# Kernel tuning notes

Measured on AMD Instinct MI355X. Metric: run time of the kernel, lower is better.

The kernel has to match this reference:

```python
import jax, jax.numpy as jnp
import numpy as np

B = 65536   # batch
F = 256     # FeatureDim
E = 8       # experts_num
D = 64      # ExpertOutDim
EPS = 1e-5  # BatchNorm eps (eval mode: running stats)


def _bn(x, g, be, m, v):
    # BatchNorm1d in eval mode
    return (x - m) * jax.lax.rsqrt(v + EPS) * g + be


def setup_inputs() -> dict:
    key = jax.random.key(0)
    ks = jax.random.split(key, 40)
    r = lambda i, s: jax.random.normal(ks[i], s, dtype=jnp.float32) * 0.05
    u = lambda i, s: jax.random.uniform(ks[i], s, dtype=jnp.float32)
    return dict(
        signal_em=jax.random.normal(ks[0], (B, F), dtype=jnp.float32),
        muti_em=jax.random.normal(ks[1], (B, F), dtype=jnp.float32),
        similarity=jax.random.uniform(ks[2], (B,), dtype=jnp.float32),
        w=u(3, ()), b=u(4, ()),
        ps_W=r(5, (F, 256)), ps_b=r(6, (256,)), ps_g=u(7, (256,)), ps_be=r(8, (256,)), ps_m=r(9, (256,)), ps_v=u(10, (256,)) + 0.5,
        pm_W=r(11, (F, 256)), pm_b=r(12, (256,)), pm_g=u(13, (256,)), pm_be=r(14, (256,)), pm_m=r(15, (256,)), pm_v=u(16, (256,)) + 0.5,
        c1_W=r(17, (2 * F, 64)), c1_b=r(18, (64,)), c1_g=u(19, (64,)), c1_be=r(20, (64,)), c1_m=r(21, (64,)), c1_v=u(22, (64,)) + 0.5,
        c2_W=r(23, (64, 64)), c2_b=r(24, (64,)), c2_g=u(25, (64,)), c2_be=r(26, (64,)), c2_m=r(27, (64,)), c2_v=u(28, (64,)) + 0.5,
        c3_W=r(29, (64, 2)), c3_b=r(30, (2,)),
        e_W1=r(31, (E, 2 * F, 256)), e_b1=r(32, (E, 256)),
        e_W2=r(33, (E, 256, D)), e_b2=r(34, (E, D)),
        s_W1=r(35, (E, E)), s_b1=r(36, (E,)), s_W2=r(37, (E, E)), s_b2=r(38, (E,)),
    )


def reference(signal_em, muti_em, similarity, w, b,
              ps_W, ps_b, ps_g, ps_be, ps_m, ps_v,
              pm_W, pm_b, pm_g, pm_be, pm_m, pm_v,
              c1_W, c1_b, c1_g, c1_be, c1_m, c1_v,
              c2_W, c2_b, c2_g, c2_be, c2_m, c2_v,
              c3_W, c3_b,
              e_W1, e_b1, e_W2, e_b2,
              s_W1, s_b1, s_W2, s_b2):
    sim_weight = similarity[:, None] * w + b                        # [B,1]
    sig = jax.nn.relu(_bn(signal_em @ ps_W + ps_b, ps_g, ps_be, ps_m, ps_v))
    sig = sim_weight * sig
    mut = jax.nn.relu(_bn(muti_em @ pm_W + pm_b, pm_g, pm_be, pm_m, pm_v))
    temp = jnp.concatenate([sig, mut], axis=1)                      # [B, 512]

    # classifier head (dropout = identity in eval mode)
    h = jax.nn.relu(_bn(temp @ c1_W + c1_b, c1_g, c1_be, c1_m, c1_v))
    h = jax.nn.relu(_bn(h @ c2_W + c2_b, c2_g, c2_be, c2_m, c2_v))
    pre_score = h @ c3_W + c3_b                                     # [B,2]

    # all E experts as one batched GEMM (Expert_net has dropout p=0)
    eh = jax.nn.relu(jnp.einsum('bf,efh->beh', temp, e_W1) + e_b1)  # [B,E,256]
    eo = jax.nn.relu(jnp.einsum('beh,ehd->bed', eh, e_W2) + e_b2)   # [B,E,64]

    # SE-style gating: avg/max pool over expert-out dim (kernel==D -> scalar)
    att_ave = eo.mean(axis=-1)                                      # [B,E]
    att_max = eo.max(axis=-1)                                       # [B,E]
    senet = lambda x: jax.nn.gelu(x @ s_W1 + s_b1, approximate=False) @ s_W2 + s_b2
    wts = jax.nn.sigmoid(senet(att_ave) + senet(att_max))           # [B,E]

    gate_out = jnp.einsum('bed,be->bd', eo, wts)                    # [B,D]
    return (gate_out, pre_score)
```

## Files before the change

### kernel.cpp

```cpp
#include <hip/hip_runtime.h>
#include <math.h>

using u32 = unsigned int;
using u16 = unsigned short;
typedef __attribute__((ext_vector_type(4))) float f4;
typedef __attribute__((ext_vector_type(4))) u32 u4;
typedef __attribute__((ext_vector_type(2))) u32 u2;
typedef __attribute__((ext_vector_type(8))) __bf16 b8;

union U4B8 { u4 u; b8 b; };

__device__ __forceinline__ u16 f2b(float x) {
  u32 u = __float_as_uint(x);
  u32 r = (u + 0x7FFFu + ((u >> 16) & 1u)) >> 16;
  return (u16)r;
}
__device__ __forceinline__ u32 pack2(float a, float b) { return (u32)f2b(a) | ((u32)f2b(b) << 16); }
__device__ __forceinline__ f4 mfma16(b8 a, b8 b, f4 c) {
  return __builtin_amdgcn_mfma_f32_16x16x32_bf16(a, b, c, 0, 0, 0);
}

#define FENCE() asm volatile("" ::: "memory")
#define RAWBAR() do { FENCE(); __builtin_amdgcn_s_barrier(); FENCE(); __builtin_amdgcn_sched_barrier(0); } while (0)
#define VMW(nlit) do { asm volatile("s_waitcnt vmcnt(" nlit ")" ::: "memory"); __builtin_amdgcn_sched_barrier(0); } while (0)
#define LGKM0() do { asm volatile("s_waitcnt lgkmcnt(0)" ::: "memory"); __builtin_amdgcn_sched_barrier(0); } while (0)
#define LBAR() do { LGKM0(); __builtin_amdgcn_s_barrier(); FENCE(); __builtin_amdgcn_sched_barrier(0); } while (0)

template <int NB>
__device__ __forceinline__ void gstage(const u16* g, u16* l, int t) {
#pragma unroll
  for (int i = 0; i < NB; i += 8192) {
    __builtin_amdgcn_global_load_lds(
        (__attribute__((address_space(1))) u32*)(g + (i >> 1) + t * 8),
        (__attribute__((address_space(3))) u32*)(l + (i >> 1) + ((t >> 6) << 9)),
        16, 0, 0);
  }
}

__global__ void prep_kernel(
    const float* __restrict__ ps_W, const float* __restrict__ ps_b, const float* __restrict__ ps_g,
    const float* __restrict__ ps_be, const float* __restrict__ ps_m, const float* __restrict__ ps_v,
    const float* __restrict__ pm_W, const float* __restrict__ pm_b, const float* __restrict__ pm_g,
    const float* __restrict__ pm_be, const float* __restrict__ pm_m, const float* __restrict__ pm_v,
    const float* __restrict__ c1_W, const float* __restrict__ c1_b, const float* __restrict__ c1_g,
    const float* __restrict__ c1_be, const float* __restrict__ c1_m, const float* __restrict__ c1_v,
    const float* __restrict__ c2_W, const float* __restrict__ c2_b, const float* __restrict__ c2_g,
    const float* __restrict__ c2_be, const float* __restrict__ c2_m, const float* __restrict__ c2_v,
    u16* __restrict__ pst, u16* __restrict__ pmt,
    u16* __restrict__ c1t, u16* __restrict__ c2t, float* __restrict__ fold)
{
  int i0 = blockIdx.x * blockDim.x + threadIdx.x;
  int stride = gridDim.x * blockDim.x;
  for (int idx = i0; idx < 65536; idx += stride) {
    int s = idx >> 14; int rem = idx & 16383;
    int n = rem >> 6, q = rem & 63;
    int k = s * 64 + (q ^ ((n & 7) << 3));
    pst[idx] = f2b(ps_W[k * 256 + n]);
    pmt[idx] = f2b(pm_W[k * 256 + n]);
  }
  for (int idx = i0; idx < 64 * 512; idx += stride) {
    int n = idx >> 9, q = idx & 511;
    int k = q ^ ((n & 7) << 3);
    c1t[idx] = f2b(c1_W[k * 64 + n]);
  }
  for (int idx = i0; idx < 64 * 64; idx += stride) {
    int n = idx >> 6, k = idx & 63;
    c2t[idx] = f2b(c2_W[k * 64 + n]);
  }
  for (int idx = i0; idx < 256; idx += stride) {
    float a = ps_g[idx] * rsqrtf(ps_v[idx] + 1e-5f);
    fold[idx] = a; fold[256 + idx] = (ps_b[idx] - ps_m[idx]) * a + ps_be[idx];
    float a2 = pm_g[idx] * rsqrtf(pm_v[idx] + 1e-5f);
    fold[512 + idx] = a2; fold[768 + idx] = (pm_b[idx] - pm_m[idx]) * a2 + pm_be[idx];
  }
  for (int idx = i0; idx < 64; idx += stride) {
    float a = c1_g[idx] * rsqrtf(c1_v[idx] + 1e-5f);
    fold[1024 + idx] = a; fold[1088 + idx] = (c1_b[idx] - c1_m[idx]) * a + c1_be[idx];
    float a2 = c2_g[idx] * rsqrtf(c2_v[idx] + 1e-5f);
    fold[1152 + idx] = a2; fold[1216 + idx] = (c2_b[idx] - c2_m[idx]) * a2 + c2_be[idx];
  }
}

__global__ __launch_bounds__(512, 4) void k1_kernel(
    const float* __restrict__ sig, const float* __restrict__ mut,
    const float* __restrict__ simil, const float* __restrict__ wS, const float* __restrict__ bS,
    const u16* __restrict__ pst, const u16* __restrict__ pmt,
    const float* __restrict__ fold, u16* __restrict__ temp,
    const float* __restrict__ e_W1, const float* __restrict__ e_W2,
    u16* __restrict__ w1t, u16* __restrict__ w2t)
{
  extern __shared__ __align__(16) u16 smk[];
  const int t = threadIdx.x;
  if (blockIdx.y == 2) {
    int i0 = blockIdx.x * 512 + t;
    const int stride = 1024 * 512;
    for (int idx = i0; idx < 8 * 256 * 512; idx += stride) {
      int e = idx >> 17; int rem = idx & 131071;
      int s = rem >> 14; int rem2 = rem & 16383;
      int n = rem2 >> 6; int q = rem2 & 63;
      int k = s * 64 + (q ^ ((n & 7) << 3));
      w1t[idx] = f2b(e_W1[e * 131072 + k * 256 + n]);
    }
    for (int idx = i0; idx < 8 * 64 * 256; idx += stride) {
      int e = idx >> 14; int rem = idx & 16383;
      int d = rem >> 8; int q = rem & 255;
      int h = q ^ ((d & 7) << 3);
      w2t[idx] = f2b(e_W2[e * 16384 + h * 64 + d]);
    }
    return;
  }
  const int w = t >> 6, l = t & 63;
  const int lr = l & 15, lk = (l >> 4) * 8, lv = (l >> 4) * 4;
  const int xoru = (l & 7) << 3;
  const int rg = w >> 1, cg = w & 1;
  const int half = blockIdx.y;
  const float* X = half ? mut : sig;
  const u16* Wt = half ? pmt : pst;
  const int rb = blockIdx.x;
  const int rg0 = rb * 64;
  const f4 ZF = {0.f, 0.f, 0.f, 0.f};
  const int myrow = rg * 16 + lr;

  f4 xr[16];
  {
    const float* xp = X + (rg0 + myrow) * 256 + lk;
#pragma unroll
    for (int c = 0; c < 8; ++c) {
      xr[2 * c]     = *(const f4*)(xp + c * 32);
      xr[2 * c + 1] = *(const f4*)(xp + c * 32 + 4);
    }
  }
  float swv = 1.f;
  if (half == 0) swv = simil[rg0 + myrow] * wS[0] + bS[0];
  gstage<32768>(Wt, smk, t);
  b8 af[8];
#pragma unroll
  for (int c = 0; c < 8; ++c) {
    U4B8 tmp;
    tmp.u[0] = pack2(xr[2 * c][0], xr[2 * c][1]);
    tmp.u[1] = pack2(xr[2 * c][2], xr[2 * c][3]);
    tmp.u[2] = pack2(xr[2 * c + 1][0], xr[2 * c + 1][1]);
    tmp.u[3] = pack2(xr[2 * c + 1][2], xr[2 * c + 1][3]);
    af[c] = tmp.b;
  }

  f4 acc[8];
#pragma unroll
  for (int i = 0; i < 8; ++i) acc[i] = ZF;

#define K1P(P, STG) do { \
    VMW("0"); RAWBAR(); \
    STG; \
    __builtin_amdgcn_s_setprio(1); \
    _Pragma("unroll") for (int kk = 0; kk < 2; ++kk) { \
      b8 bf[8]; \
      _Pragma("unroll") for (int nf = 0; nf < 8; ++nf) \
        bf[nf] = *(const b8*)(smk + ((P) & 1) * 16384 + (cg * 128 + nf * 16 + lr) * 64 + ((kk * 32 + lk) ^ xoru)); \
      _Pragma("unroll") for (int nf = 0; nf < 8; ++nf) \
        acc[nf] = mfma16(bf[nf], af[(P) * 2 + kk], acc[nf]); \
    } \
    __builtin_amdgcn_s_setprio(0); \
  } while (0)

  K1P(0, gstage<32768>(Wt + 16384, smk + 16384, t));
  K1P(1, gstage<32768>(Wt + 32768, smk, t));
  K1P(2, gstage<32768>(Wt + 49152, smk + 16384, t));
  K1P(3, (void)0);
#undef K1P

#pragma unroll
  for (int nf = 0; nf < 8; ++nf) {
    int col = cg * 128 + nf * 16 + lv;
    const f4 al = *(const f4*)(fold + half * 512 + col);
    const f4 be = *(const f4*)(fold + half * 512 + 256 + col);
    float v0 = fmaxf(acc[nf][0] * al[0] + be[0], 0.f) * swv;
    float v1 = fmaxf(acc[nf][1] * al[1] + be[1], 0.f) * swv;
    float v2 = fmaxf(acc[nf][2] * al[2] + be[2], 0.f) * swv;
    float v3 = fmaxf(acc[nf][3] * al[3] + be[3], 0.f) * swv;
    u2 pv; pv[0] = pack2(v0, v1); pv[1] = pack2(v2, v3);
    int st = col >> 6;
    int kin = col & 63;
    int q = kin ^ ((myrow & 7) << 3);
    *(u2*)(smk + st * 4096 + myrow * 64 + q) = pv;
  }
  LBAR();
  {
    u16* dst = temp + (rb >> 1) * 65536 + half * 32768 + (rb & 1) * 4096;
#pragma unroll
    for (int st = 0; st < 4; ++st) {
      u4 v = *(const u4*)(smk + st * 4096 + t * 8);
      *(u4*)(dst + st * 8192 + t * 8) = v;
    }
  }
}

__global__ __launch_bounds__(512, 2) void k2_kernel(
    u16* __restrict__ temp, const u16* __restrict__ w1t, const u16* __restrict__ w2t,
    const u16* __restrict__ c1t, const u16* __restrict__ c2t,
    const float* __restrict__ fold,
    const float* __restrict__ c3W, const float* __restrict__ c3B,
    const float* __restrict__ eb1, const float* __restrict__ eb2,
    const float* __restrict__ sW1, const float* __restrict__ sB1,
    const float* __restrict__ sW2, const float* __restrict__ sB2,
    float* __restrict__ outp)
{
  extern __shared__ __align__(16) u16 sm[];
  u16* smW  = sm;
  u16* smE  = sm + 32768;
  u16* smR2 = sm + 49152;
  float* attA  = (float*)(sm + 65536);
  float* attM  = attA + 1024;
  float* wtsb  = attM + 1024;
  float* c3sm  = wtsb + 1024;
  float* eb1sm = c3sm + 136;
  float* eb2sm = eb1sm + 2048;

  const int t = threadIdx.x, w = t >> 6, l = t & 63;
  const int lr = l & 15, lk = (l >> 4) * 8, lv = (l >> 4) * 4;
  const int xoru = (l & 7) << 3;
  const int rg = w >> 1, cg = w & 1;
  const int rg0 = blockIdx.x * 128;
  const f4 ZF = {0.f, 0.f, 0.f, 0.f};
  u16* tempE = temp + blockIdx.x * 65536;

  b8 af[16][2];

#define AFLOAD(R) { \
    _Pragma("unroll") for (int c8 = 0; c8 < 8; ++c8) { \
      _Pragma("unroll") for (int mi = 0; mi < 2; ++mi) \
        af[(R) * 8 + c8][mi] = *(const b8*)(smE + (c8 >> 1) * 8192 + (rg * 32 + mi * 16 + lr) * 64 + ((((c8 & 1) * 32) + lk) ^ xoru)); \
    } }

  {
    for (int z = t; z < 2048; z += 512) attA[z] = 0.f;
    f4 rEb1 = *(const f4*)(eb1 + t * 4);
    f4 rEb2 = ZF; if (t < 128) rEb2 = *(const f4*)(eb2 + t * 4);
    float rC3 = 0.f; if (t < 128) rC3 = c3W[t]; else if (t < 130) rC3 = c3B[t - 128];
    u4 rC2 = *(const u4*)(c2t + (t >> 3) * 64 + (t & 7) * 8);

    gstage<65536>(tempE, smE, t);
    gstage<65536>(c1t, smW, t);
    *(f4*)(eb1sm + t * 4) = rEb1;
    if (t < 128) *(f4*)(eb2sm + t * 4) = rEb2;
    if (t < 130) c3sm[t] = rC3;
    VMW("8"); RAWBAR();
    AFLOAD(0);
    asm volatile("s_waitcnt lgkmcnt(0)" ::: "memory");
    RAWBAR();
    gstage<65536>(tempE + 32768, smE, t);
    VMW("8"); RAWBAR();
    f4 ah[2][2] = {{ZF, ZF}, {ZF, ZF}};
#define HPART(R) { \
    __builtin_amdgcn_s_setprio(1); \
    _Pragma("unroll") for (int c8 = 0; c8 < 8; ++c8) { \
      _Pragma("unroll") for (int nf = 0; nf < 2; ++nf) { \
        b8 ch = *(const b8*)(smW + (cg * 32 + nf * 16 + lr) * 512 + ((((R) * 8 + c8) * 32 + lk) ^ xoru)); \
        _Pragma("unroll") for (int mi = 0; mi < 2; ++mi) \
          ah[nf][mi] = mfma16(ch, af[(R) * 8 + c8][mi], ah[nf][mi]); \
      } } \
    __builtin_amdgcn_s_setprio(0); }
    HPART(0)
    VMW("0"); RAWBAR();
    AFLOAD(1);
    HPART(1)
#undef HPART
    asm volatile("s_waitcnt lgkmcnt(0)" ::: "memory");
    RAWBAR();
    u16* h1b = smE;
    u16* c2sm = smR2;
    u16* h2b = smR2 + 4608;
#pragma unroll
    for (int nf = 0; nf < 2; ++nf) {
      int col = cg * 32 + nf * 16 + lv;
      const f4 av1 = *(const f4*)(fold + 1024 + col);
      const f4 bv1 = *(const f4*)(fold + 1088 + col);
#pragma unroll
      for (int mi = 0; mi < 2; ++mi) {
        int row = rg * 32 + mi * 16 + lr;
        u2 pv;
        pv[0] = pack2(fmaxf(ah[nf][mi][0] * av1[0] + bv1[0], 0.f), fmaxf(ah[nf][mi][1] * av1[1] + bv1[1], 0.f));
        pv[1] = pack2(fmaxf(ah[nf][mi][2] * av1[2] + bv1[2], 0.f), fmaxf(ah[nf][mi][3] * av1[3] + bv1[3], 0.f));
        *(u2*)(h1b + row * 72 + col) = pv;
      }
    }
    *(u4*)(c2sm + (t >> 3) * 72 + (t & 7) * 8) = rC2;
    LBAR();
    f4 a2[2][2] = {{ZF, ZF}, {ZF, ZF}};
#pragma unroll
    for (int kk = 0; kk < 2; ++kk) {
      b8 hf[2], cf[2];
#pragma unroll
      for (int mi = 0; mi < 2; ++mi)
        hf[mi] = *(const b8*)(h1b + (rg * 32 + mi * 16 + lr) * 72 + kk * 32 + lk);
#pragma unroll
      for (int nf = 0; nf < 2; ++nf)
        cf[nf] = *(const b8*)(c2sm + (cg * 32 + nf * 16 + lr) * 72 + kk * 32 + lk);
#pragma unroll
      for (int mi = 0; mi < 2; ++mi)
#pragma unroll
        for (int nf = 0; nf < 2; ++nf)
          a2[mi][nf] = mfma16(cf[nf], hf[mi], a2[mi][nf]);
    }
#pragma unroll
    for (int nf = 0; nf < 2; ++nf) {
      int col = cg * 32 + nf * 16 + lv;
      const f4 av2 = *(const f4*)(fold + 1152 + col);
      const f4 bv2 = *(const f4*)(fold + 1216 + col);
#pragma unroll
      for (int mi = 0; mi < 2; ++mi) {
        int row = rg * 32 + mi * 16 + lr;
        u2 pv;
        pv[0] = pack2(fmaxf(a2[mi][nf][0] * av2[0] + bv2[0], 0.f), fmaxf(a2[mi][nf][1] * av2[1] + bv2[1], 0.f));
        pv[1] = pack2(fmaxf(a2[mi][nf][2] * av2[2] + bv2[2], 0.f), fmaxf(a2[mi][nf][3] * av2[3] + bv2[3], 0.f));
        *(u2*)(h2b + row * 72 + col) = pv;
      }
    }
    LBAR();
    if (t < 256) {
      int row = t >> 1, c = t & 1;
      float s_ = c3sm[128 + c];
#pragma unroll
      for (int j = 0; j < 8; ++j) {
        u4 hv = *(const u4*)(h2b + row * 72 + j * 8);
#pragma unroll
        for (int q = 0; q < 4; ++q) {
          float lo = __uint_as_float(hv[q] << 16);
          float hi = __uint_as_float(hv[q] & 0xffff0000u);
          s_ += lo * c3sm[(j * 8 + q * 2) * 2 + c];
          s_ += hi * c3sm[(j * 8 + q * 2 + 1) * 2 + c];
        }
      }
      outp[4194304 + (rg0 + row) * 2 + c] = s_;
    }
    RAWBAR();
    gstage<32768>(w1t, smW, t);
  }

#define MPH(P, NW, ...) do { \
    VMW(NW); RAWBAR(); \
    __VA_ARGS__; \
    __builtin_amdgcn_s_setprio(1); \
    _Pragma("unroll") for (int kk = 0; kk < 2; ++kk) { \
      b8 bfA[4], bfB[4]; \
      _Pragma("unroll") for (int nf = 0; nf < 4; ++nf) \
        bfA[nf] = *(const b8*)(smW + ((P) & 1) * 16384 + (cg * 64 + nf * 16 + lr) * 64 + ((kk * 32 + lk) ^ xoru)); \
      _Pragma("unroll") for (int nf = 0; nf < 4; ++nf) \
        bfB[nf] = *(const b8*)(smW + ((P) & 1) * 16384 + 8192 + (cg * 64 + nf * 16 + lr) * 64 + ((kk * 32 + lk) ^ xoru)); \
      _Pragma("unroll") for (int nf = 0; nf < 4; ++nf) \
        _Pragma("unroll") for (int mi = 0; mi < 2; ++mi) \
          acc[nf][mi] = mfma16(bfA[nf], af[(P) * 2 + kk][mi], acc[nf][mi]); \
      _Pragma("unroll") for (int nf = 0; nf < 4; ++nf) \
        _Pragma("unroll") for (int mi = 0; mi < 2; ++mi) \
          acc[4 + nf][mi] = mfma16(bfB[nf], af[(P) * 2 + kk][mi], acc[4 + nf][mi]); \
    } \
    __builtin_amdgcn_s_setprio(0); \
  } while (0)

#define EHEPI(E, H, DST) { \
    _Pragma("unroll") for (int nf = 0; nf < 4; ++nf) { \
      int colL = cg * 64 + nf * 16 + lv; \
      const f4 bv = *(const f4*)(eb1sm + (E) * 256 + (H) * 128 + colL); \
      _Pragma("unroll") for (int mi = 0; mi < 2; ++mi) { \
        int row = rg * 32 + mi * 16 + lr; \
        f4 a_ = acc[(H) * 4 + nf][mi]; \
        u2 pv; \
        pv[0] = pack2(fmaxf(a_[0] + bv[0], 0.f), fmaxf(a_[1] + bv[1], 0.f)); \
        pv[1] = pack2(fmaxf(a_[2] + bv[2], 0.f), fmaxf(a_[3] + bv[3], 0.f)); \
        *(u2*)((DST) + row * 128 + (colL ^ xoru)) = pv; \
      } } }

#define G2ALL() do { \
    __builtin_amdgcn_s_setprio(1); \
    _Pragma("unroll") for (int kq = 0; kq < 8; ++kq) { \
      const u16* ebase = (kq < 4) ? smE : (smW + 16384); \
      b8 wf[2], ef[2]; \
      _Pragma("unroll") for (int nf = 0; nf < 2; ++nf) \
        wf[nf] = *(const b8*)(smR2 + (cg * 32 + nf * 16 + lr) * 256 + ((kq * 32 + lk) ^ xoru)); \
      _Pragma("unroll") for (int mi = 0; mi < 2; ++mi) \
        ef[mi] = *(const b8*)(ebase + (rg * 32 + mi * 16 + lr) * 128 + ((((kq & 3) * 32) + lk) ^ xoru)); \
      _Pragma("unroll") for (int mi = 0; mi < 2; ++mi) \
        _Pragma("unroll") for (int nf = 0; nf < 2; ++nf) \
          e2[mi][nf] = mfma16(wf[nf], ef[mi], e2[mi][nf]); \
    } \
    __builtin_amdgcn_s_setprio(0); \
  } while (0)

#define EXPERT(E, NWP0, NWG2) { \
    const u16* w1E = w1t + (E) * 131072; \
    f4 acc[8][2]; \
    _Pragma("unroll") for (int nf = 0; nf < 8; ++nf) \
      _Pragma("unroll") for (int mi = 0; mi < 2; ++mi) acc[nf][mi] = ZF; \
    MPH(0, NWP0, gstage<32768>(w1E + 1 * 16384, smW + 16384, t)); \
    MPH(1, "0",  gstage<32768>(w1E + 2 * 16384, smW, t)); \
    MPH(2, "0",  gstage<32768>(w1E + 3 * 16384, smW + 16384, t)); \
    MPH(3, "0",  gstage<32768>(w1E + 4 * 16384, smW, t)); \
    MPH(4, "0",  gstage<32768>(w1E + 5 * 16384, smW + 16384, t)); \
    MPH(5, "0",  gstage<32768>(w1E + 6 * 16384, smW, t)); \
    MPH(6, "0",  { gstage<32768>(w1E + 7 * 16384, smW + 16384, t); \
                   gstage<32768>(w2t + (E) * 16384, smR2, t); }); \
    MPH(7, "4",  { if ((E) < 7) gstage<32768>(w1t + ((E) + 1) * 131072, smW, t); }); \
    EHEPI(E, 0, smE) \
    RAWBAR();  \
    EHEPI(E, 1, smW + 16384) \
    VMW(NWG2); LBAR();  \
    f4 e2[2][2]; \
    e2[0][0] = ZF; e2[0][1] = ZF; e2[1][0] = ZF; e2[1][1] = ZF; \
    G2ALL(); \
     \
    _Pragma("unroll") for (int mi = 0; mi < 2; ++mi) { \
      int row = rg * 32 + mi * 16 + lr; \
      float s_ = 0.f, mx = 0.f; \
      _Pragma("unroll") for (int nf = 0; nf < 2; ++nf) { \
        int d0 = cg * 32 + nf * 16 + lv; \
        const f4 bv2 = *(const f4*)(eb2sm + (E) * 64 + d0); \
        float v0 = fmaxf(e2[mi][nf][0] + bv2[0], 0.f); \
        float v1 = fmaxf(e2[mi][nf][1] + bv2[1], 0.f); \
        float v2 = fmaxf(e2[mi][nf][2] + bv2[2], 0.f); \
        float v3 = fmaxf(e2[mi][nf][3] + bv2[3], 0.f); \
        s_ += v0 + v1 + v2 + v3; \
        mx = fmaxf(mx, fmaxf(fmaxf(v0, v1), fmaxf(v2, v3))); \
        u2 pv; pv[0] = pack2(v0, v1); pv[1] = pack2(v2, v3); \
        *(u2*)(tempE + (E) * 8192 + row * 64 + d0) = pv; \
      } \
      s_ += __shfl_xor(s_, 16); s_ += __shfl_xor(s_, 32); \
      mx = fmaxf(mx, __shfl_xor(mx, 16)); mx = fmaxf(mx, __shfl_xor(mx, 32)); \
      if (l < 16) { \
        atomicAdd(attA + row * 8 + (E), s_); \
        atomicMax((unsigned int*)(attM + row * 8 + (E)), __float_as_uint(mx)); \
      } \
    } \
  }

  EXPERT(0, "0", "4")
  EXPERT(1, "4", "4")
  EXPERT(2, "4", "4")
  EXPERT(3, "4", "4")
  EXPERT(4, "4", "4")
  EXPERT(5, "4", "4")
  EXPERT(6, "4", "4")
  EXPERT(7, "4", "0")
#undef EXPERT
#undef MPH
#undef EHEPI
#undef G2ALL

  VMW("0");
  LBAR();
  if (t < 128) {
    float xa[8], xm[8], ga[8], gm[8];
#pragma unroll
    for (int j = 0; j < 8; ++j) {
      xa[j] = attA[t * 8 + j] * 0.015625f;
      xm[j] = attM[t * 8 + j];
    }
#pragma unroll
    for (int j = 0; j < 8; ++j) {
      float a1 = sB1[j], a2 = sB1[j];
#pragma unroll
      for (int i = 0; i < 8; ++i) { float wv = sW1[i * 8 + j]; a1 += xa[i] * wv; a2 += xm[i] * wv; }
      ga[j] = 0.5f * a1 * (1.f + erff(a1 * 0.70710678118654752f));
      gm[j] = 0.5f * a2 * (1.f + erff(a2 * 0.70710678118654752f));
    }
#pragma unroll
    for (int j = 0; j < 8; ++j) {
      float o1 = sB2[j], o2 = sB2[j];
#pragma unroll
      for (int i = 0; i < 8; ++i) { float wv = sW2[i * 8 + j]; o1 += ga[i] * wv; o2 += gm[i] * wv; }
      float z = o1 + o2;
      wtsb[t * 8 + j] = 1.f / (1.f + expf(-z));
    }
  }
  LBAR();
  {
    int grow = t >> 2, gd0 = (t & 3) * 16;
    float wv[8];
#pragma unroll
    for (int e2_ = 0; e2_ < 8; ++e2_) wv[e2_] = wtsb[grow * 8 + e2_];
    float g[16];
#pragma unroll
    for (int j = 0; j < 16; ++j) g[j] = 0.f;
#pragma unroll
    for (int e2_ = 0; e2_ < 8; ++e2_) {
      const u16* wsE = tempE + e2_ * 8192 + grow * 64 + gd0;
      u4 qa = *(const u4*)(wsE); u4 qb = *(const u4*)(wsE + 8);
#pragma unroll
      for (int q = 0; q < 4; ++q) {
        g[2 * q + 0] += wv[e2_] * __uint_as_float(qa[q] << 16);
        g[2 * q + 1] += wv[e2_] * __uint_as_float(qa[q] & 0xffff0000u);
        g[8 + 2 * q + 0] += wv[e2_] * __uint_as_float(qb[q] << 16);
        g[8 + 2 * q + 1] += wv[e2_] * __uint_as_float(qb[q] & 0xffff0000u);
      }
    }
    float* op = outp + (rg0 + grow) * 64 + gd0;
    f4 o0 = {g[0], g[1], g[2], g[3]}, o1 = {g[4], g[5], g[6], g[7]};
    f4 o2 = {g[8], g[9], g[10], g[11]}, o3 = {g[12], g[13], g[14], g[15]};
    *(f4*)op = o0; *(f4*)(op + 4) = o1; *(f4*)(op + 8) = o2; *(f4*)(op + 12) = o3;
  }
}

extern "C" void kernel_launch(void* const* d_in, const int* in_sizes, int n_in,
                              void* d_out, int out_size, void* d_ws, size_t ws_size,
                              hipStream_t stream) {
  const float* signal = (const float*)d_in[0];
  const float* muti   = (const float*)d_in[1];
  const float* simil  = (const float*)d_in[2];
  const float* wS     = (const float*)d_in[3];
  const float* bS     = (const float*)d_in[4];
  const float* ps_W = (const float*)d_in[5];  const float* ps_b = (const float*)d_in[6];
  const float* ps_g = (const float*)d_in[7];  const float* ps_be = (const float*)d_in[8];
  const float* ps_m = (const float*)d_in[9];  const float* ps_v = (const float*)d_in[10];
  const float* pm_W = (const float*)d_in[11]; const float* pm_b = (const float*)d_in[12];
  const float* pm_g = (const float*)d_in[13]; const float* pm_be = (const float*)d_in[14];
  const float* pm_m = (const float*)d_in[15]; const float* pm_v = (const float*)d_in[16];
  const float* c1_W = (const float*)d_in[17]; const float* c1_b = (const float*)d_in[18];
  const float* c1_g = (const float*)d_in[19]; const float* c1_be = (const float*)d_in[20];
  const float* c1_m = (const float*)d_in[21]; const float* c1_v = (const float*)d_in[22];
  const float* c2_W = (const float*)d_in[23]; const float* c2_b = (const float*)d_in[24];
  const float* c2_g = (const float*)d_in[25]; const float* c2_be = (const float*)d_in[26];
  const float* c2_m = (const float*)d_in[27]; const float* c2_v = (const float*)d_in[28];
  const float* c3_W = (const float*)d_in[29]; const float* c3_b = (const float*)d_in[30];
  const float* e_W1 = (const float*)d_in[31]; const float* e_b1 = (const float*)d_in[32];
  const float* e_W2 = (const float*)d_in[33]; const float* e_b2 = (const float*)d_in[34];
  const float* s_W1 = (const float*)d_in[35]; const float* s_b1 = (const float*)d_in[36];
  const float* s_W2 = (const float*)d_in[37]; const float* s_b2 = (const float*)d_in[38];

  char* ws = (char*)d_ws;
  u16* temp = (u16*)ws;
  u16* w1t  = (u16*)(ws + 67108864);
  u16* w2t  = (u16*)(ws + 69206016);
  u16* pst  = (u16*)(ws + 69468160);
  u16* pmt  = (u16*)(ws + 69599232);
  u16* c1t  = (u16*)(ws + 69730304);
  u16* c2t  = (u16*)(ws + 69795840);
  float* fold = (float*)(ws + 69804032);
  float* outp = (float*)d_out;

  prep_kernel<<<dim3(256), dim3(256), 0, stream>>>(
      ps_W, ps_b, ps_g, ps_be, ps_m, ps_v, pm_W, pm_b, pm_g, pm_be, pm_m, pm_v,
      c1_W, c1_b, c1_g, c1_be, c1_m, c1_v, c2_W, c2_b, c2_g, c2_be, c2_m, c2_v,
      pst, pmt, c1t, c2t, fold);
  k1_kernel<<<dim3(1024, 3), dim3(512), 65536, stream>>>(
      signal, muti, simil, wS, bS, pst, pmt, fold, temp, e_W1, e_W2, w1t, w2t);
  k2_kernel<<<dim3(512), dim3(512), 154144, stream>>>(
      temp, w1t, w2t, c1t, c2t, fold, c3_W, c3_b, e_b1, e_b2, s_W1, s_b1, s_W2, s_b2, outp);
}
```

Measured before the change: 261.7 us.

## Shrink k2 to 64-row 256-thread blocks with smaller LDS footprint

Restructures the main expert kernel from 128-row, 512-thread blocks using about 154KB of LDS to 64-row, 256-thread blocks using about 72KB, doubling the grid to 1024 blocks. The temp layout, the w1t swizzle layout and the staging step sizes change to match. All phases now share a single LDS region, and expert biases are read from global memory instead of LDS. The aim is more resident blocks per CU and better latency hiding. In exchange, the cross-expert prefetch overlap and the multi-stage vmcnt pipelining are dropped (every phase waits for vmcnt 0), and each block re-reads the expert weights for only half as many rows.

```diff
diff --git a/kernel.cpp b/kernel.cpp
--- a/kernel.cpp
+++ b/kernel.cpp
@@ -26,10 +26,10 @@
 #define LGKM0() do { asm volatile("s_waitcnt lgkmcnt(0)" ::: "memory"); __builtin_amdgcn_sched_barrier(0); } while (0)
 #define LBAR() do { LGKM0(); __builtin_amdgcn_s_barrier(); FENCE(); __builtin_amdgcn_sched_barrier(0); } while (0)
 
-template <int NB>
+template <int NB, int STEP>
 __device__ __forceinline__ void gstage(const u16* g, u16* l, int t) {
 #pragma unroll
-  for (int i = 0; i < NB; i += 8192) {
+  for (int i = 0; i < NB; i += STEP) {
     __builtin_amdgcn_global_load_lds(
         (__attribute__((address_space(1))) u32*)(g + (i >> 1) + t * 8),
         (__attribute__((address_space(3))) u32*)(l + (i >> 1) + ((t >> 6) << 9)),
@@ -96,9 +96,10 @@
     const int stride = 1024 * 512;
     for (int idx = i0; idx < 8 * 256 * 512; idx += stride) {
       int e = idx >> 17; int rem = idx & 131071;
-      int s = rem >> 14; int rem2 = rem & 16383;
-      int n = rem2 >> 6; int q = rem2 & 63;
-      int k = s * 64 + (q ^ ((n & 7) << 3));
+      int S = rem >> 13; int rem2 = rem & 8191;
+      int nl = rem2 >> 6; int q = rem2 & 63;
+      int n = (S & 1) * 128 + nl;
+      int k = (S >> 1) * 64 + (q ^ ((nl & 7) << 3));
       w1t[idx] = f2b(e_W1[e * 131072 + k * 256 + n]);
     }
     for (int idx = i0; idx < 8 * 64 * 256; idx += stride) {
@@ -132,7 +133,7 @@
   }
   float swv = 1.f;
   if (half == 0) swv = simil[rg0 + myrow] * wS[0] + bS[0];
-  gstage<32768>(Wt, smk, t);
+  gstage<32768, 8192>(Wt, smk, t);
   b8 af[8];
 #pragma unroll
   for (int c = 0; c < 8; ++c) {
@@ -148,9 +149,9 @@
 #pragma unroll
   for (int i = 0; i < 8; ++i) acc[i] = ZF;
 
-#define K1P(P, STG) do { \
+#define K1P(P, ...) do { \
     VMW("0"); RAWBAR(); \
-    STG; \
+    __VA_ARGS__; \
     __builtin_amdgcn_s_setprio(1); \
     _Pragma("unroll") for (int kk = 0; kk < 2; ++kk) { \
       b8 bf[8]; \
@@ -162,9 +163,9 @@
     __builtin_amdgcn_s_setprio(0); \
   } while (0)
 
-  K1P(0, gstage<32768>(Wt + 16384, smk + 16384, t));
-  K1P(1, gstage<32768>(Wt + 32768, smk, t));
-  K1P(2, gstage<32768>(Wt + 49152, smk + 16384, t));
+  K1P(0, (gstage<32768, 8192>(Wt + 16384, smk + 16384, t)));
+  K1P(1, (gstage<32768, 8192>(Wt + 32768, smk, t)));
+  K1P(2, (gstage<32768, 8192>(Wt + 49152, smk + 16384, t)));
   K1P(3, (void)0);
 #undef K1P
 
@@ -185,16 +186,16 @@
   }
   LBAR();
   {
-    u16* dst = temp + (rb >> 1) * 65536 + half * 32768 + (rb & 1) * 4096;
+    u16* dst = temp + rb * 32768 + half * 16384;
 #pragma unroll
     for (int st = 0; st < 4; ++st) {
       u4 v = *(const u4*)(smk + st * 4096 + t * 8);
-      *(u4*)(dst + st * 8192 + t * 8) = v;
-    }
-  }
-}
-
-__global__ __launch_bounds__(512, 2) void k2_kernel(
+      *(u4*)(dst + st * 4096 + t * 8) = v;
+    }
+  }
+}
+
+__global__ __launch_bounds__(256, 2) void k2_kernel(
     u16* __restrict__ temp, const u16* __restrict__ w1t, const u16* __restrict__ w2t,
     const u16* __restrict__ c1t, const u16* __restrict__ c2t,
     const float* __restrict__ fold,
@@ -206,69 +207,61 @@
 {
   extern __shared__ __align__(16) u16 sm[];
   u16* smW  = sm;
-  u16* smE  = sm + 32768;
-  u16* smR2 = sm + 49152;
-  float* attA  = (float*)(sm + 65536);
-  float* attM  = attA + 1024;
-  float* wtsb  = attM + 1024;
-  float* c3sm  = wtsb + 1024;
-  float* eb1sm = c3sm + 136;
-  float* eb2sm = eb1sm + 2048;
+  float* attA = (float*)(sm + 32768);
+  float* attM = attA + 512;
+  float* wtsb = attM + 512;
+  float* c3sm = wtsb + 512;
 
   const int t = threadIdx.x, w = t >> 6, l = t & 63;
   const int lr = l & 15, lk = (l >> 4) * 8, lv = (l >> 4) * 4;
   const int xoru = (l & 7) << 3;
   const int rg = w >> 1, cg = w & 1;
-  const int rg0 = blockIdx.x * 128;
+  const int rg0 = blockIdx.x * 64;
   const f4 ZF = {0.f, 0.f, 0.f, 0.f};
-  u16* tempE = temp + blockIdx.x * 65536;
+  u16* tempE = temp + blockIdx.x * 32768;
 
   b8 af[16][2];
 
 #define AFLOAD(R) { \
     _Pragma("unroll") for (int c8 = 0; c8 < 8; ++c8) { \
       _Pragma("unroll") for (int mi = 0; mi < 2; ++mi) \
-        af[(R) * 8 + c8][mi] = *(const b8*)(smE + (c8 >> 1) * 8192 + (rg * 32 + mi * 16 + lr) * 64 + ((((c8 & 1) * 32) + lk) ^ xoru)); \
+        af[(R) * 8 + c8][mi] = *(const b8*)(smW + (R) * 16384 + (c8 >> 1) * 4096 + (rg * 32 + mi * 16 + lr) * 64 + ((((c8 & 1) * 32) + lk) ^ xoru)); \
     } }
 
   {
-    for (int z = t; z < 2048; z += 512) attA[z] = 0.f;
-    f4 rEb1 = *(const f4*)(eb1 + t * 4);
-    f4 rEb2 = ZF; if (t < 128) rEb2 = *(const f4*)(eb2 + t * 4);
+    for (int z = t; z < 1024; z += 256) attA[z] = 0.f;
     float rC3 = 0.f; if (t < 128) rC3 = c3W[t]; else if (t < 130) rC3 = c3B[t - 128];
-    u4 rC2 = *(const u4*)(c2t + (t >> 3) * 64 + (t & 7) * 8);
-
-    gstage<65536>(tempE, smE, t);
-    gstage<65536>(c1t, smW, t);
-    *(f4*)(eb1sm + t * 4) = rEb1;
-    if (t < 128) *(f4*)(eb2sm + t * 4) = rEb2;
+    u4 rC2a = *(const u4*)(c2t + (t >> 3) * 64 + (t & 7) * 8);
+    u4 rC2b = *(const u4*)(c2t + ((t + 256) >> 3) * 64 + ((t + 256) & 7) * 8);
+
+    gstage<32768, 4096>(tempE, smW, t);
+    gstage<32768, 4096>(tempE + 16384, smW + 16384, t);
     if (t < 130) c3sm[t] = rC3;
     VMW("8"); RAWBAR();
     AFLOAD(0);
-    asm volatile("s_waitcnt lgkmcnt(0)" ::: "memory");
-    RAWBAR();
-    gstage<65536>(tempE + 32768, smE, t);
-    VMW("8"); RAWBAR();
+    VMW("0");
+    LGKM0(); RAWBAR();
+    AFLOAD(1);
+    LGKM0(); RAWBAR();
+    gstage<65536, 4096>(c1t, smW, t);
+    VMW("0"); RAWBAR();
     f4 ah[2][2] = {{ZF, ZF}, {ZF, ZF}};
-#define HPART(R) { \
-    __builtin_amdgcn_s_setprio(1); \
-    _Pragma("unroll") for (int c8 = 0; c8 < 8; ++c8) { \
-      _Pragma("unroll") for (int nf = 0; nf < 2; ++nf) { \
-        b8 ch = *(const b8*)(smW + (cg * 32 + nf * 16 + lr) * 512 + ((((R) * 8 + c8) * 32 + lk) ^ xoru)); \
-        _Pragma("unroll") for (int mi = 0; mi < 2; ++mi) \
-          ah[nf][mi] = mfma16(ch, af[(R) * 8 + c8][mi], ah[nf][mi]); \
-      } } \
-    __builtin_amdgcn_s_setprio(0); }
-    HPART(0)
-    VMW("0"); RAWBAR();
-    AFLOAD(1);
-    HPART(1)
-#undef HPART
-    asm volatile("s_waitcnt lgkmcnt(0)" ::: "memory");
-    RAWBAR();
-    u16* h1b = smE;
-    u16* c2sm = smR2;
-    u16* h2b = smR2 + 4608;
+    __builtin_amdgcn_s_setprio(1);
+#pragma unroll
+    for (int c8 = 0; c8 < 16; ++c8) {
+#pragma unroll
+      for (int nf = 0; nf < 2; ++nf) {
+        b8 ch = *(const b8*)(smW + (cg * 32 + nf * 16 + lr) * 512 + ((c8 * 32 + lk) ^ xoru));
+#pragma unroll
+        for (int mi = 0; mi < 2; ++mi)
+          ah[nf][mi] = mfma16(ch, af[c8][mi], ah[nf][mi]);
+      }
+    }
+    __builtin_amdgcn_s_setprio(0);
+    LGKM0(); RAWBAR();
+    u16* h1b  = smW;
+    u16* c2sm = smW + 4608;
+    u16* h2b  = smW + 9216;
 #pragma unroll
     for (int nf = 0; nf < 2; ++nf) {
       int col = cg * 32 + nf * 16 + lv;
@@ -283,7 +276,8 @@
         *(u2*)(h1b + row * 72 + col) = pv;
       }
     }
-    *(u4*)(c2sm + (t >> 3) * 72 + (t & 7) * 8) = rC2;
+    *(u4*)(c2sm + (t >> 3) * 72 + (t & 7) * 8) = rC2a;
+    *(u4*)(c2sm + ((t + 256) >> 3) * 72 + ((t + 256) & 7) * 8) = rC2b;
     LBAR();
     f4 a2[2][2] = {{ZF, ZF}, {ZF, ZF}};
 #pragma unroll
@@ -316,7 +310,7 @@
       }
     }
     LBAR();
-    if (t < 256) {
+    if (t < 128) {
       int row = t >> 1, c = t & 1;
       float s_ = c3sm[128 + c];
 #pragma unroll
@@ -333,86 +327,106 @@
       outp[4194304 + (rg0 + row) * 2 + c] = s_;
     }
     RAWBAR();
-    gstage<32768>(w1t, smW, t);
-  }
-
-#define MPH(P, NW, ...) do { \
-    VMW(NW); RAWBAR(); \
+    gstage<32768, 4096>(w1t, smW, t);
+  }
+
+#define MPH(P, ...) do { \
+    VMW("0"); RAWBAR(); \
     __VA_ARGS__; \
     __builtin_amdgcn_s_setprio(1); \
     _Pragma("unroll") for (int kk = 0; kk < 2; ++kk) { \
-      b8 bfA[4], bfB[4]; \
-      _Pragma("unroll") for (int nf = 0; nf < 4; ++nf) \
-        bfA[nf] = *(const b8*)(smW + ((P) & 1) * 16384 + (cg * 64 + nf * 16 + lr) * 64 + ((kk * 32 + lk) ^ xoru)); \
-      _Pragma("unroll") for (int nf = 0; nf < 4; ++nf) \
-        bfB[nf] = *(const b8*)(smW + ((P) & 1) * 16384 + 8192 + (cg * 64 + nf * 16 + lr) * 64 + ((kk * 32 + lk) ^ xoru)); \
-      _Pragma("unroll") for (int nf = 0; nf < 4; ++nf) \
-        _Pragma("unroll") for (int mi = 0; mi < 2; ++mi) \
-          acc[nf][mi] = mfma16(bfA[nf], af[(P) * 2 + kk][mi], acc[nf][mi]); \
-      _Pragma("unroll") for (int nf = 0; nf < 4; ++nf) \
-        _Pragma("unroll") for (int mi = 0; mi < 2; ++mi) \
-          acc[4 + nf][mi] = mfma16(bfB[nf], af[(P) * 2 + kk][mi], acc[4 + nf][mi]); \
+      b8 bf[8]; \
+      _Pragma("unroll") for (int nf = 0; nf < 8; ++nf) \
+        bf[nf] = *(const b8*)(smW + ((P) & 1) * 16384 + cg * 8192 + (nf * 16 + lr) * 64 + ((kk * 32 + lk) ^ xoru)); \
+      _Pragma("unroll") for (int nf = 0; nf < 8; ++nf) \
+        acc[nf] = mfma16(bf[nf], af[(P) * 2 + kk], acc[nf]); \
     } \
     __builtin_amdgcn_s_setprio(0); \
   } while (0)
 
-#define EHEPI(E, H, DST) { \
-    _Pragma("unroll") for (int nf = 0; nf < 4; ++nf) { \
-      int colL = cg * 64 + nf * 16 + lv; \
-      const f4 bv = *(const f4*)(eb1sm + (E) * 256 + (H) * 128 + colL); \
-      _Pragma("unroll") for (int mi = 0; mi < 2; ++mi) { \
-        int row = rg * 32 + mi * 16 + lr; \
-        f4 a_ = acc[(H) * 4 + nf][mi]; \
+#define G32(SRC, DST) gstage<32768, 4096>((SRC), (DST), t)
+
+#define EXPERT(E) { \
+    const u16* w1E = w1t + (E) * 131072; \
+    f4 acc[8]; \
+    _Pragma("unroll") for (int nf = 0; nf < 8; ++nf) acc[nf] = ZF; \
+    MPH(0, G32(w1E + 1 * 16384, smW + 16384)); \
+    MPH(1, G32(w1E + 2 * 16384, smW)); \
+    MPH(2, G32(w1E + 3 * 16384, smW + 16384)); \
+    MPH(3, G32(w1E + 4 * 16384, smW)); \
+    MPH(4, G32(w1E + 5 * 16384, smW + 16384)); \
+    MPH(5, G32(w1E + 6 * 16384, smW)); \
+    MPH(6, G32(w1E + 7 * 16384, smW + 16384)); \
+    MPH(7, G32(w2t + (E) * 16384, smW)); \
+    VMW("0"); RAWBAR();  \
+     \
+    _Pragma("unroll") for (int nf = 0; nf < 8; ++nf) { \
+      int col = cg * 128 + nf * 16 + lv; \
+      const f4 bv = *(const f4*)(eb1 + (E) * 256 + col); \
+      int row = rg * 32 + lr;   \
+      (void)row; \
+      _Pragma("unroll") for (int mi = 0; mi < 1; ++mi) { } \
+      { \
+        int r0 = rg * 32 + lr; \
+        f4 a_ = acc[nf]; \
         u2 pv; \
         pv[0] = pack2(fmaxf(a_[0] + bv[0], 0.f), fmaxf(a_[1] + bv[1], 0.f)); \
         pv[1] = pack2(fmaxf(a_[2] + bv[2], 0.f), fmaxf(a_[3] + bv[3], 0.f)); \
-        *(u2*)((DST) + row * 128 + (colL ^ xoru)) = pv; \
-      } } }
-
-#define G2ALL() do { \
+        *(u2*)(smW + 16384 + r0 * 256 + (col ^ xoru)) = pv; \
+      } \
+    } \
+    LBAR(); \
+  }
+
+#undef EXPERT
+#define EXPERT(E) { \
+    const u16* w1E = w1t + (E) * 131072; \
+    f4 acc[8][2]; \
+    _Pragma("unroll") for (int nf = 0; nf < 8; ++nf) \
+      _Pragma("unroll") for (int mi = 0; mi < 2; ++mi) acc[nf][mi] = ZF; \
+    MPH2(0, G32(w1E + 1 * 16384, smW + 16384)); \
+    MPH2(1, G32(w1E + 2 * 16384, smW)); \
+    MPH2(2, G32(w1E + 3 * 16384, smW + 16384)); \
+    MPH2(3, G32(w1E + 4 * 16384, smW)); \
+    MPH2(4, G32(w1E + 5 * 16384, smW + 16384)); \
+    MPH2(5, G32(w1E + 6 * 16384, smW)); \
+    MPH2(6, G32(w1E + 7 * 16384, smW + 16384)); \
+    MPH2(7, G32(w2t + (E) * 16384, smW)); \
+    VMW("0"); RAWBAR();  \
+     \
+    _Pragma("unroll") for (int nf = 0; nf < 8; ++nf) { \
+      int col = cg * 128 + nf * 16 + lv; \
+      const f4 bv = *(const f4*)(eb1 + (E) * 256 + col); \
+      _Pragma("unroll") for (int mi = 0; mi < 2; ++mi) { \
+        int row = rg * 32 + mi * 16 + lr; \
+        f4 a_ = acc[nf][mi]; \
+        u2 pv; \
+        pv[0] = pack2(fmaxf(a_[0] + bv[0], 0.f), fmaxf(a_[1] + bv[1], 0.f)); \
+        pv[1] = pack2(fmaxf(a_[2] + bv[2], 0.f), fmaxf(a_[3] + bv[3], 0.f)); \
+        *(u2*)(smW + 16384 + row * 256 + (col ^ xoru)) = pv; \
+      } } \
+    LBAR();  \
+    f4 e2[2][2]; \
+    e2[0][0] = ZF; e2[0][1] = ZF; e2[1][0] = ZF; e2[1][1] = ZF; \
     __builtin_amdgcn_s_setprio(1); \
     _Pragma("unroll") for (int kq = 0; kq < 8; ++kq) { \
-      const u16* ebase = (kq < 4) ? smE : (smW + 16384); \
       b8 wf[2], ef[2]; \
       _Pragma("unroll") for (int nf = 0; nf < 2; ++nf) \
-        wf[nf] = *(const b8*)(smR2 + (cg * 32 + nf * 16 + lr) * 256 + ((kq * 32 + lk) ^ xoru)); \
+        wf[nf] = *(const b8*)(smW + (cg * 32 + nf * 16 + lr) * 256 + ((kq * 32 + lk) ^ xoru)); \
       _Pragma("unroll") for (int mi = 0; mi < 2; ++mi) \
-        ef[mi] = *(const b8*)(ebase + (rg * 32 + mi * 16 + lr) * 128 + ((((kq & 3) * 32) + lk) ^ xoru)); \
+        ef[mi] = *(const b8*)(smW + 16384 + (rg * 32 + mi * 16 + lr) * 256 + ((kq * 32 + lk) ^ xoru)); \
       _Pragma("unroll") for (int mi = 0; mi < 2; ++mi) \
         _Pragma("unroll") for (int nf = 0; nf < 2; ++nf) \
           e2[mi][nf] = mfma16(wf[nf], ef[mi], e2[mi][nf]); \
     } \
     __builtin_amdgcn_s_setprio(0); \
-  } while (0)
-
-#define EXPERT(E, NWP0, NWG2) { \
-    const u16* w1E = w1t + (E) * 131072; \
-    f4 acc[8][2]; \
-    _Pragma("unroll") for (int nf = 0; nf < 8; ++nf) \
-      _Pragma("unroll") for (int mi = 0; mi < 2; ++mi) acc[nf][mi] = ZF; \
-    MPH(0, NWP0, gstage<32768>(w1E + 1 * 16384, smW + 16384, t)); \
-    MPH(1, "0",  gstage<32768>(w1E + 2 * 16384, smW, t)); \
-    MPH(2, "0",  gstage<32768>(w1E + 3 * 16384, smW + 16384, t)); \
-    MPH(3, "0",  gstage<32768>(w1E + 4 * 16384, smW, t)); \
-    MPH(4, "0",  gstage<32768>(w1E + 5 * 16384, smW + 16384, t)); \
-    MPH(5, "0",  gstage<32768>(w1E + 6 * 16384, smW, t)); \
-    MPH(6, "0",  { gstage<32768>(w1E + 7 * 16384, smW + 16384, t); \
-                   gstage<32768>(w2t + (E) * 16384, smR2, t); }); \
-    MPH(7, "4",  { if ((E) < 7) gstage<32768>(w1t + ((E) + 1) * 131072, smW, t); }); \
-    EHEPI(E, 0, smE) \
-    RAWBAR();  \
-    EHEPI(E, 1, smW + 16384) \
-    VMW(NWG2); LBAR();  \
-    f4 e2[2][2]; \
-    e2[0][0] = ZF; e2[0][1] = ZF; e2[1][0] = ZF; e2[1][1] = ZF; \
-    G2ALL(); \
      \
     _Pragma("unroll") for (int mi = 0; mi < 2; ++mi) { \
       int row = rg * 32 + mi * 16 + lr; \
       float s_ = 0.f, mx = 0.f; \
       _Pragma("unroll") for (int nf = 0; nf < 2; ++nf) { \
         int d0 = cg * 32 + nf * 16 + lv; \
-        const f4 bv2 = *(const f4*)(eb2sm + (E) * 64 + d0); \
+        const f4 bv2 = *(const f4*)(eb2 + (E) * 64 + d0); \
         float v0 = fmaxf(e2[mi][nf][0] + bv2[0], 0.f); \
         float v1 = fmaxf(e2[mi][nf][1] + bv2[1], 0.f); \
         float v2 = fmaxf(e2[mi][nf][2] + bv2[2], 0.f); \
@@ -420,7 +434,7 @@
         s_ += v0 + v1 + v2 + v3; \
         mx = fmaxf(mx, fmaxf(fmaxf(v0, v1), fmaxf(v2, v3))); \
         u2 pv; pv[0] = pack2(v0, v1); pv[1] = pack2(v2, v3); \
-        *(u2*)(tempE + (E) * 8192 + row * 64 + d0) = pv; \
+        *(u2*)(tempE + (E) * 4096 + row * 64 + d0) = pv; \
       } \
       s_ += __shfl_xor(s_, 16); s_ += __shfl_xor(s_, 32); \
       mx = fmaxf(mx, __shfl_xor(mx, 16)); mx = fmaxf(mx, __shfl_xor(mx, 32)); \
@@ -429,24 +443,41 @@
         atomicMax((unsigned int*)(attM + row * 8 + (E)), __float_as_uint(mx)); \
       } \
     } \
-  }
-
-  EXPERT(0, "0", "4")
-  EXPERT(1, "4", "4")
-  EXPERT(2, "4", "4")
-  EXPERT(3, "4", "4")
-  EXPERT(4, "4", "4")
-  EXPERT(5, "4", "4")
-  EXPERT(6, "4", "4")
-  EXPERT(7, "4", "0")
+    RAWBAR();  \
+    if ((E) < 7) G32(w1t + ((E) + 1) * 131072, smW); \
+  }
+
+#define MPH2(P, ...) do { \
+    VMW("0"); RAWBAR(); \
+    __VA_ARGS__; \
+    __builtin_amdgcn_s_setprio(1); \
+    _Pragma("unroll") for (int kk = 0; kk < 2; ++kk) { \
+      b8 bf[8]; \
+      _Pragma("unroll") for (int nf = 0; nf < 8; ++nf) \
+        bf[nf] = *(const b8*)(smW + ((P) & 1) * 16384 + cg * 8192 + (nf * 16 + lr) * 64 + ((kk * 32 + lk) ^ xoru)); \
+      _Pragma("unroll") for (int nf = 0; nf < 8; ++nf) \
+        _Pragma("unroll") for (int mi = 0; mi < 2; ++mi) \
+          acc[nf][mi] = mfma16(bf[nf], af[(P) * 2 + kk][mi], acc[nf][mi]); \
+    } \
+    __builtin_amdgcn_s_setprio(0); \
+  } while (0)
+
+  EXPERT(0)
+  EXPERT(1)
+  EXPERT(2)
+  EXPERT(3)
+  EXPERT(4)
+  EXPERT(5)
+  EXPERT(6)
+  EXPERT(7)
 #undef EXPERT
 #undef MPH
-#undef EHEPI
-#undef G2ALL
+#undef MPH2
+#undef G32
 
   VMW("0");
   LBAR();
-  if (t < 128) {
+  if (t < 64) {
     float xa[8], xm[8], ga[8], gm[8];
 #pragma unroll
     for (int j = 0; j < 8; ++j) {
@@ -481,7 +512,7 @@
     for (int j = 0; j < 16; ++j) g[j] = 0.f;
 #pragma unroll
     for (int e2_ = 0; e2_ < 8; ++e2_) {
-      const u16* wsE = tempE + e2_ * 8192 + grow * 64 + gd0;
+      const u16* wsE = tempE + e2_ * 4096 + grow * 64 + gd0;
       u4 qa = *(const u4*)(wsE); u4 qb = *(const u4*)(wsE + 8);
 #pragma unroll
       for (int q = 0; q < 4; ++q) {
@@ -541,6 +572,6 @@
       pst, pmt, c1t, c2t, fold);
   k1_kernel<<<dim3(1024, 3), dim3(512), 65536, stream>>>(
       signal, muti, simil, wS, bS, pst, pmt, fold, temp, e_W1, e_W2, w1t, w2t);
-  k2_kernel<<<dim3(512), dim3(512), 154144, stream>>>(
+  k2_kernel<<<dim3(1024), dim3(256), 72224, stream>>>(
       temp, w1t, w2t, c1t, c2t, fold, c3_W, c3_b, e_b1, e_b2, s_W1, s_b1, s_W2, s_b2, outp);
 }
```

Result: slower. 297.2 us (+13.6%).
